# Performance work log

Measured on AMD Instinct MI355X. Metric: run time of the kernel, lower is better.

Reference implementation:

```python
import jax, jax.numpy as jnp
import numpy as np
from jax import lax

EPS = 1e-08
PAD = 1  # kernel_size // 2 for k=3


def setup_inputs() -> dict:
    key = jax.random.key(0)
    k1, k2, k3, k4 = jax.random.split(key, 4)
    B, Cin, Cout, H, W, K, S = 16, 256, 256, 64, 64, 3, 512
    x = jax.random.normal(k1, (B, Cin, H, W), dtype=jnp.float32)
    style = jax.random.normal(k2, (B, S), dtype=jnp.float32)
    mod_weight = jax.random.normal(k3, (Cin, S), dtype=jnp.float32)
    mod_bias = jnp.zeros((Cin,), dtype=jnp.float32)
    weight = jax.random.normal(k4, (1, Cout, Cin, K, K), dtype=jnp.float32)
    bias = jnp.zeros((1, Cout, 1, 1), dtype=jnp.float32)
    return {"x": x, "style": style, "mod_weight": mod_weight,
            "mod_bias": mod_bias, "weight": weight, "bias": bias}


def reference(x, style, mod_weight, mod_bias, weight, bias):
    # EqualizedLinear modulation (lr_mul = 1.0): s[b, cin]
    s = style @ mod_weight.T + mod_bias  # [B, Cin]
    # per-sample modulated weights: [B, Cout, Cin, K, K]
    w = weight * s[:, None, :, None, None]
    # demodulation: rsqrt of sum over (Cin, K, K)
    demod = lax.rsqrt(jnp.sum(w * w, axis=(2, 3, 4)) + EPS)  # [B, Cout]
    w = w * demod[:, :, None, None, None]

    # per-sample conv2d (groups=B equivalent) via vmap over batch
    def conv_one(xb, wb):
        # xb: [Cin, H, W], wb: [Cout, Cin, K, K]
        return lax.conv_general_dilated(
            xb[None], wb, window_strides=(1, 1),
            padding=[(PAD, PAD), (PAD, PAD)],
            dimension_numbers=("NCHW", "OIHW", "NCHW"))[0]

    out = jax.vmap(conv_one)(x, w)  # [B, Cout, H, W]
    return out + bias
```

## Files before the change

### kernel.cpp

```cpp
#include <hip/hip_runtime.h>

#define EPS 1e-8f
#define THREADS 512

typedef __attribute__((ext_vector_type(8))) short short8;
typedef __attribute__((ext_vector_type(4))) float f32x4;
typedef __attribute__((ext_vector_type(8))) unsigned short u16x8;

static __device__ __forceinline__ unsigned short f2bf(float f) {
  unsigned int u = __float_as_uint(f);
  u += 0x7FFF + ((u >> 16) & 1);
  return (unsigned short)(u >> 16);
}

__global__ void k_prep(const float* __restrict__ style, const float* __restrict__ mw,
                       const float* __restrict__ mb, float* __restrict__ s_out,
                       const float* __restrict__ weight, float* __restrict__ wsq,
                       unsigned short* __restrict__ wbf) {
  __shared__ float sm[2304];
  int t = threadIdx.x;
  if (blockIdx.x < 16) {
    int b = blockIdx.x;
    sm[t]       = style[b*512 + t];
    sm[t + 256] = style[b*512 + 256 + t];
    __syncthreads();
    const float4* row = (const float4*)(mw + (size_t)t*512);
    float acc = 0.f;
#pragma unroll 4
    for (int i = 0; i < 128; ++i) {
      float4 m = row[i];
      acc += m.x*sm[4*i] + m.y*sm[4*i+1] + m.z*sm[4*i+2] + m.w*sm[4*i+3];
    }
    s_out[b*256 + t] = acc + mb[t];
  } else {
    int co = blockIdx.x - 16;
    for (int q = t; q < 576; q += 256)
      *(float4*)&sm[q*4] = *(const float4*)(weight + (size_t)co*2304 + q*4);
    __syncthreads();
    int ci = t;
    int c = ci >> 6, cil = ci & 63;
    int base = ((co*128 + cil*2) ^ ((co & 7) << 4)) >> 1;
    float sum = 0.f;
#pragma unroll
    for (int r = 0; r < 9; ++r) {
      float v = sm[ci*9 + r];
      sum += v*v;
      wbf[(size_t)(c*9 + r)*16384 + base] = f2bf(v);
    }
    wsq[co*256 + ci] = sum;
  }
}

__global__ void k_demod(const float* __restrict__ s, const float* __restrict__ wsq,
                        float* __restrict__ dm) {
  int b = blockIdx.x, t = threadIdx.x;
  __shared__ float s2[256];
  float sv = s[b*256 + t];
  s2[t] = sv*sv;
  __syncthreads();
  const float4* row = (const float4*)(wsq + (size_t)t*256);
  float acc = 0.f;
#pragma unroll 4
  for (int i = 0; i < 64; ++i) {
    float4 q = row[i];
    acc += q.x*s2[4*i] + q.y*s2[4*i+1] + q.z*s2[4*i+2] + q.w*s2[4*i+3];
  }
  dm[b*256 + t] = rsqrtf(acc + EPS);
}

__global__ void k_pad(const float* __restrict__ x, const float* __restrict__ s,
                      unsigned short* __restrict__ xp) {
  int bid = blockIdx.x;
  int b = bid / 66, gh = bid - b*66;
  int t = threadIdx.x;
  size_t rowbase = (size_t)(b*66 + gh) * (66*256);
  u16x8* rp = (u16x8*)(xp + rowbase);
  if (gh == 0 || gh == 65) {
    u16x8 z = (u16x8)0;
    for (int q = t; q < 2112; q += 256) rp[q] = z;
    return;
  }
  int h = gh - 1;
  __shared__ float sl[256];
  __shared__ unsigned short xl[64*256];
  sl[t] = s[b*256 + t];
  __syncthreads();
  int w4 = (t & 15) * 4, o0 = t >> 4;
#pragma unroll
  for (int p = 0; p < 2; ++p) {
    int oct = o0 + p*16;
    u16x8 outv[4];
#pragma unroll
    for (int j = 0; j < 8; ++j) {
      int ci = oct*8 + j;
      float4 v = *(const float4*)(x + ((size_t)(b*256 + ci)*64 + h)*64 + w4);
      float sc = sl[ci];
      outv[0][j] = (short)f2bf(v.x * sc);
      outv[1][j] = (short)f2bf(v.y * sc);
      outv[2][j] = (short)f2bf(v.z * sc);
      outv[3][j] = (short)f2bf(v.w * sc);
    }
#pragma unroll
    for (int k = 0; k < 4; ++k) {
      int w = w4 + k;
      int byte = w*512 + ((oct ^ (w & 31)) << 4);
      *(u16x8*)((char*)xl + byte) = outv[k];
    }
  }
  __syncthreads();
  u16x8 z = (u16x8)0;
  if (t < 32) rp[t] = z;
  else if (t < 64) rp[65*32 + (t - 32)] = z;
  for (int q = t; q < 2048; q += 256) {
    int w2 = q >> 5, slot = q & 31;
    u16x8 v = *(const u16x8*)((char*)xl + w2*512 + ((slot ^ (w2 & 31)) << 4));
    rp[(w2 + 1)*32 + slot] = v;
  }
}

__global__ __launch_bounds__(512, 4)
void k_conv(const unsigned short* __restrict__ xp, const unsigned short* __restrict__ wbf,
            const float* __restrict__ dm, const float* __restrict__ bias,
            float* __restrict__ out) {
  __shared__ unsigned short x_lds[4*66*64];
  __shared__ unsigned short w_lds[256*64];

  const int tid = threadIdx.x;
  const int lane = tid & 63;
  const int wave = tid >> 6;
  const int bid = (blockIdx.x & 7)*64 + (blockIdx.x >> 3);
  const int b = bid >> 5;
  const int h0 = (bid & 31) * 2;
  const int wm = wave >> 1, wn = wave & 1;
  const int l15 = lane & 15, lk = lane >> 4;

  f32x4 acc[4][4];
#pragma unroll
  for (int m = 0; m < 4; ++m)
#pragma unroll
    for (int f = 0; f < 4; ++f) acc[m][f] = (f32x4)0.f;

  for (int c = 0; c < 4; ++c) {
    __syncthreads();
    {
      int cb = c*64;
#pragma unroll
      for (int it = 0; it < 5; ++it) {
        int q = it*THREADS + tid;
        if (q < 2112) {
          int hw = q >> 3;
          int hl = hw / 66, w = hw - hl*66;
          int slot = (q & 7) ^ (hw & 7);
          const unsigned short* src =
              xp + (size_t)((b*66 + h0 + hl)*66 + w)*256 + cb + slot*8;
          __builtin_amdgcn_global_load_lds(
              (const __attribute__((address_space(1))) void*)src,
              (__attribute__((address_space(3))) void*)&x_lds[(size_t)q*8],
              16, 0, 0);
        }
      }
    }
    for (int r = 0; r < 9; ++r) {
      if (r) __syncthreads();
      {
        const unsigned short* wsrc = wbf + (size_t)(c*9 + r)*16384;
#pragma unroll
        for (int it = 0; it < 4; ++it) {
          int q = it*THREADS + tid;
          __builtin_amdgcn_global_load_lds(
              (const __attribute__((address_space(1))) void*)(wsrc + (size_t)q*8),
              (__attribute__((address_space(3))) void*)&w_lds[(size_t)q*8],
              16, 0, 0);
        }
      }
      __syncthreads();
      int dh = r / 3, dw = r - dh*3;
#pragma unroll
      for (int kh = 0; kh < 2; ++kh) {
        int cio = (kh*32 + lk*8)*2;
        short8 a[4], bf[4];
#pragma unroll
        for (int m = 0; m < 4; ++m) {
          int co = wm*64 + m*16 + l15;
          int byte = (co*128 + cio) ^ ((co & 7) << 4);
          a[m] = *(const short8*)((const char*)w_lds + byte);
        }
#pragma unroll
        for (int f = 0; f < 4; ++f) {
          int row = (wn + dh)*66 + (f*16 + l15 + dw);
          int byte = (row*128 + cio) ^ ((row & 7) << 4);
          bf[f] = *(const short8*)((const char*)x_lds + byte);
        }
#pragma unroll
        for (int m = 0; m < 4; ++m)
#pragma unroll
          for (int f = 0; f < 4; ++f)
            acc[m][f] = __builtin_amdgcn_mfma_f32_16x16x32_bf16(a[m], bf[f], acc[m][f], 0, 0, 0);
      }
    }
  }

  int colane = (lane >> 4) * 4;
#pragma unroll
  for (int m = 0; m < 4; ++m) {
    int cob = wm*64 + m*16 + colane;
    float4 d4 = *(const float4*)&dm[b*256 + cob];
    float4 b4 = *(const float4*)&bias[cob];
    int h = h0 + wn;
#pragma unroll
    for (int f = 0; f < 4; ++f) {
      int wc = f*16 + l15;
      float* op = out + ((size_t)(b*256 + cob)*64 + h)*64 + wc;
      op[0]     = acc[m][f][0] * d4.x + b4.x;
      op[4096]  = acc[m][f][1] * d4.y + b4.y;
      op[8192]  = acc[m][f][2] * d4.z + b4.z;
      op[12288] = acc[m][f][3] * d4.w + b4.w;
    }
  }
}

extern "C" void kernel_launch(void* const* d_in, const int* in_sizes, int n_in,
                              void* d_out, int out_size, void* d_ws, size_t ws_size,
                              hipStream_t stream) {
  const float* x      = (const float*)d_in[0];
  const float* style  = (const float*)d_in[1];
  const float* mw     = (const float*)d_in[2];
  const float* mb     = (const float*)d_in[3];
  const float* weight = (const float*)d_in[4];
  const float* bias   = (const float*)d_in[5];
  float* out = (float*)d_out;

  char* ws = (char*)d_ws;
  float* s_buf        = (float*)(ws);
  float* wsq          = (float*)(ws + 16384);
  float* dmod         = (float*)(ws + 16384 + 262144);
  unsigned short* wbf = (unsigned short*)(ws + 294912);
  unsigned short* xpd = (unsigned short*)(ws + 294912 + 1179648);

  k_prep<<<272, 256, 0, stream>>>(style, mw, mb, s_buf, weight, wsq, wbf);
  k_demod<<<16, 256, 0, stream>>>(s_buf, wsq, dmod);
  k_pad<<<16*66, 256, 0, stream>>>(x, s_buf, xpd);
  k_conv<<<512, 512, 0, stream>>>(xpd, wbf, dmod, bias, out);
}
```

Baseline: 248.6 us.

## Enlarge conv tile to four rows and double-buffer weight staging

Each conv block now covers four output rows instead of two, so every weight slab loaded into LDS feeds twice as many MFMAs. Weight tiles are double-buffered: the next tap's slab is prefetched while the current one is being consumed, which drops one barrier per tap. MFMA sections are also wrapped in s_setprio. The cost is a doubled accumulator count, which lowers occupancy (launch bounds 512,2). The grid halves to 256 blocks, which may underfill the MI355X's CUs.

```diff
diff --git a/kernel.cpp b/kernel.cpp
--- a/kernel.cpp
+++ b/kernel.cpp
@@ -118,84 +118,97 @@
   }
 }
 
-__global__ __launch_bounds__(512, 4)
+__global__ __launch_bounds__(512, 2)
 void k_conv(const unsigned short* __restrict__ xp, const unsigned short* __restrict__ wbf,
             const float* __restrict__ dm, const float* __restrict__ bias,
             float* __restrict__ out) {
-  __shared__ unsigned short x_lds[4*66*64];
-  __shared__ unsigned short w_lds[256*64];
+  __shared__ unsigned short x_lds[6*66*64];
+  __shared__ unsigned short w_lds[2][256*64];
 
   const int tid = threadIdx.x;
   const int lane = tid & 63;
   const int wave = tid >> 6;
-  const int bid = (blockIdx.x & 7)*64 + (blockIdx.x >> 3);
-  const int b = bid >> 5;
-  const int h0 = (bid & 31) * 2;
+  const int b = blockIdx.x >> 4;
+  const int h0 = (blockIdx.x & 15) * 4;
   const int wm = wave >> 1, wn = wave & 1;
   const int l15 = lane & 15, lk = lane >> 4;
 
-  f32x4 acc[4][4];
+  f32x4 acc[4][8];
 #pragma unroll
   for (int m = 0; m < 4; ++m)
 #pragma unroll
-    for (int f = 0; f < 4; ++f) acc[m][f] = (f32x4)0.f;
+    for (int f = 0; f < 8; ++f) acc[m][f] = (f32x4)0.f;
+
+  auto stage_x = [&](int c) {
+    int cb = c*64;
+#pragma unroll
+    for (int it = 0; it < 7; ++it) {
+      int q = it*THREADS + tid;
+      if (q < 3168) {
+        int hw = q >> 3;
+        int hl = hw / 66, w = hw - hl*66;
+        int slot = (q & 7) ^ (hw & 7);
+        const unsigned short* src =
+            xp + (size_t)((b*66 + h0 + hl)*66 + w)*256 + cb + slot*8;
+        __builtin_amdgcn_global_load_lds(
+            (const __attribute__((address_space(1))) void*)src,
+            (__attribute__((address_space(3))) void*)&x_lds[(size_t)q*8],
+            16, 0, 0);
+      }
+    }
+  };
+  auto stage_w = [&](int p, int buf) {
+    const unsigned short* wsrc = wbf + (size_t)p*16384;
+#pragma unroll
+    for (int it = 0; it < 4; ++it) {
+      int q = it*THREADS + tid;
+      __builtin_amdgcn_global_load_lds(
+          (const __attribute__((address_space(1))) void*)(wsrc + (size_t)q*8),
+          (__attribute__((address_space(3))) void*)&w_lds[buf][(size_t)q*8],
+          16, 0, 0);
+    }
+  };
+
+  stage_x(0);
+  stage_w(0, 0);
+  __syncthreads();
 
   for (int c = 0; c < 4; ++c) {
-    __syncthreads();
-    {
-      int cb = c*64;
-#pragma unroll
-      for (int it = 0; it < 5; ++it) {
-        int q = it*THREADS + tid;
-        if (q < 2112) {
-          int hw = q >> 3;
-          int hl = hw / 66, w = hw - hl*66;
-          int slot = (q & 7) ^ (hw & 7);
-          const unsigned short* src =
-              xp + (size_t)((b*66 + h0 + hl)*66 + w)*256 + cb + slot*8;
-          __builtin_amdgcn_global_load_lds(
-              (const __attribute__((address_space(1))) void*)src,
-              (__attribute__((address_space(3))) void*)&x_lds[(size_t)q*8],
-              16, 0, 0);
-        }
-      }
-    }
     for (int r = 0; r < 9; ++r) {
-      if (r) __syncthreads();
-      {
-        const unsigned short* wsrc = wbf + (size_t)(c*9 + r)*16384;
-#pragma unroll
-        for (int it = 0; it < 4; ++it) {
-          int q = it*THREADS + tid;
-          __builtin_amdgcn_global_load_lds(
-              (const __attribute__((address_space(1))) void*)(wsrc + (size_t)q*8),
-              (__attribute__((address_space(3))) void*)&w_lds[(size_t)q*8],
-              16, 0, 0);
-        }
-      }
-      __syncthreads();
+      int p = c*9 + r;
+      if (p < 35) stage_w(p + 1, (p + 1) & 1);
+      const unsigned short* wb = w_lds[p & 1];
       int dh = r / 3, dw = r - dh*3;
 #pragma unroll
       for (int kh = 0; kh < 2; ++kh) {
-        int cio = (kh*32 + lk*8)*2;
-        short8 a[4], bf[4];
+        int cio = kh*64 + lk*16;
+        short8 a[4], bf[8];
 #pragma unroll
         for (int m = 0; m < 4; ++m) {
           int co = wm*64 + m*16 + l15;
           int byte = (co*128 + cio) ^ ((co & 7) << 4);
-          a[m] = *(const short8*)((const char*)w_lds + byte);
+          a[m] = *(const short8*)((const char*)wb + byte);
         }
 #pragma unroll
-        for (int f = 0; f < 4; ++f) {
-          int row = (wn + dh)*66 + (f*16 + l15 + dw);
+        for (int f = 0; f < 8; ++f) {
+          int row = (wn*2 + (f >> 2) + dh)*66 + ((f & 3)*16 + l15 + dw);
           int byte = (row*128 + cio) ^ ((row & 7) << 4);
           bf[f] = *(const short8*)((const char*)x_lds + byte);
         }
+        __builtin_amdgcn_s_setprio(1);
 #pragma unroll
         for (int m = 0; m < 4; ++m)
 #pragma unroll
-          for (int f = 0; f < 4; ++f)
+          for (int f = 0; f < 8; ++f)
             acc[m][f] = __builtin_amdgcn_mfma_f32_16x16x32_bf16(a[m], bf[f], acc[m][f], 0, 0, 0);
+        __builtin_amdgcn_s_setprio(0);
+      }
+      if (r == 8) {
+        __syncthreads();
+        if (c < 3) stage_x(c + 1);
+        __syncthreads();
+      } else {
+        __syncthreads();
       }
     }
   }
@@ -206,10 +219,10 @@
     int cob = wm*64 + m*16 + colane;
     float4 d4 = *(const float4*)&dm[b*256 + cob];
     float4 b4 = *(const float4*)&bias[cob];
-    int h = h0 + wn;
-#pragma unroll
-    for (int f = 0; f < 4; ++f) {
-      int wc = f*16 + l15;
+#pragma unroll
+    for (int f = 0; f < 8; ++f) {
+      int h = h0 + wn*2 + (f >> 2);
+      int wc = (f & 3)*16 + l15;
       float* op = out + ((size_t)(b*256 + cob)*64 + h)*64 + wc;
       op[0]     = acc[m][f][0] * d4.x + b4.x;
       op[4096]  = acc[m][f][1] * d4.y + b4.y;
@@ -240,5 +253,5 @@
   k_prep<<<272, 256, 0, stream>>>(style, mw, mb, s_buf, weight, wsq, wbf);
   k_demod<<<16, 256, 0, stream>>>(s_buf, wsq, dmod);
   k_pad<<<16*66, 256, 0, stream>>>(x, s_buf, xpd);
-  k_conv<<<512, 512, 0, stream>>>(xpd, wbf, dmod, bias, out);
-}
+  k_conv<<<256, 512, 0, stream>>>(xpd, wbf, dmod, bias, out);
+}
```

Result: faster. 224.3 us (-9.8%).
